# Optimization experiments

Measured on AMD Instinct MI355X. Metric: run time of the kernel, lower is better.

Reference implementation:

```python
import jax, jax.numpy as jnp
import numpy as np

CHUNK = 512  # tile size along N; keeps per-step [B,CHUNK,M] tile ~64 MB, never builds full [B,N,M]


def setup_inputs() -> dict:
    key = jax.random.key(0)
    k1, k2 = jax.random.split(key)
    xyz1 = jax.random.normal(k1, (4, 8192, 3), dtype=jnp.float32)
    xyz2 = jax.random.normal(k2, (4, 8192, 3), dtype=jnp.float32)
    return {"xyz1": xyz1, "xyz2": xyz2}


def _chamfer(xyz1, xyz2):
    # xyz1: [B,N,3], xyz2: [B,M,3]
    B, N, _ = xyz1.shape
    M = xyz2.shape[1]
    K = N // CHUNK
    x1_chunks = xyz1.reshape(B, K, CHUNK, 3).transpose(1, 0, 2, 3)  # [K,B,C,3]

    def step(carry, x1k):
        best_d2, best_i2, start = carry  # running mins for xyz2 -> xyz1 direction
        # squared distances for this tile: [B,C,M]
        d = jnp.sum((x1k[:, :, None, :] - xyz2[:, None, :, :]) ** 2, axis=-1)
        # xyz1 -> xyz2: min over M
        d1 = jnp.min(d, axis=2)                              # [B,C]
        i1 = jnp.argmin(d, axis=2).astype(jnp.int32)         # [B,C]
        # xyz2 -> xyz1: partial min over this chunk of N
        dc = jnp.min(d, axis=1)                              # [B,M]
        ic = jnp.argmin(d, axis=1).astype(jnp.int32) + start # [B,M], global index
        upd = dc < best_d2
        best_d2 = jnp.where(upd, dc, best_d2)
        best_i2 = jnp.where(upd, ic, best_i2)
        return (best_d2, best_i2, start + CHUNK), (d1, i1)

    init = (jnp.full((B, M), jnp.inf, dtype=xyz1.dtype),
            jnp.zeros((B, M), dtype=jnp.int32),
            jnp.int32(0))
    (dist2, idx2, _), (d1s, i1s) = jax.lax.scan(step, init, x1_chunks)
    dist1 = d1s.transpose(1, 0, 2).reshape(B, N)
    idx1 = i1s.transpose(1, 0, 2).reshape(B, N)
    return dist1, dist2, idx1, idx2


def reference(xyz1, xyz2):
    # Matches ChamferDistance.forward: (dist1, dist2, idx1, idx2),
    # squared nearest-neighbor distances and int32 argmin indices.
    return _chamfer(xyz1, xyz2)
```

## Files before the change

### kernel.cpp

```cpp
#include <hip/hip_runtime.h>
#include <math.h>


#define QPT 4
#define BLK 256
#define QPB (QPT*BLK)

#define LOADF8(J) do {                                                        \
    f0 = sv4[8*(J)+0]; f1 = sv4[8*(J)+1]; f2 = sv4[8*(J)+2];                  \
    f3 = sv4[8*(J)+3]; f4 = sv4[8*(J)+4]; f5 = sv4[8*(J)+5];                  \
    f6 = sv4[8*(J)+6]; f7 = sv4[8*(J)+7];                                     \
} while (0)

#define EMIN8(AX, AY, AZ, MOUT) do {                                          \
    float d0 = fmaf(AX, f0.x, fmaf(AY, f0.y, fmaf(AZ, f0.z, f0.w)));          \
    float d1 = fmaf(AX, f1.x, fmaf(AY, f1.y, fmaf(AZ, f1.z, f1.w)));          \
    float d2 = fmaf(AX, f2.x, fmaf(AY, f2.y, fmaf(AZ, f2.z, f2.w)));          \
    float d3 = fmaf(AX, f3.x, fmaf(AY, f3.y, fmaf(AZ, f3.z, f3.w)));          \
    float d4 = fmaf(AX, f4.x, fmaf(AY, f4.y, fmaf(AZ, f4.z, f4.w)));          \
    float d5 = fmaf(AX, f5.x, fmaf(AY, f5.y, fmaf(AZ, f5.z, f5.w)));          \
    float d6 = fmaf(AX, f6.x, fmaf(AY, f6.y, fmaf(AZ, f6.z, f6.w)));          \
    float d7 = fmaf(AX, f7.x, fmaf(AY, f7.y, fmaf(AZ, f7.z, f7.w)));          \
    float t0 = fminf(fminf(d0, d1), d2);                                      \
    float t1 = fminf(fminf(d3, d4), d5);                                      \
    float t2 = fminf(fminf(d6, d7), t0);                                      \
    MOUT = fminf(t1, t2);                                                     \
} while (0)

#define DMIN8(QX, QY, QZ, MOUT) do {                                          \
    float dx, dy, dz;                                                         \
    dx = QX - f0.x; dy = QY - f0.y; dz = QZ - f0.z;                           \
    float d0 = fmaf(dx, dx, fmaf(dy, dy, dz * dz));                           \
    dx = QX - f1.x; dy = QY - f1.y; dz = QZ - f1.z;                           \
    float d1 = fmaf(dx, dx, fmaf(dy, dy, dz * dz));                           \
    dx = QX - f2.x; dy = QY - f2.y; dz = QZ - f2.z;                           \
    float d2 = fmaf(dx, dx, fmaf(dy, dy, dz * dz));                           \
    dx = QX - f3.x; dy = QY - f3.y; dz = QZ - f3.z;                           \
    float d3 = fmaf(dx, dx, fmaf(dy, dy, dz * dz));                           \
    dx = QX - f4.x; dy = QY - f4.y; dz = QZ - f4.z;                           \
    float d4 = fmaf(dx, dx, fmaf(dy, dy, dz * dz));                           \
    dx = QX - f5.x; dy = QY - f5.y; dz = QZ - f5.z;                           \
    float d5 = fmaf(dx, dx, fmaf(dy, dy, dz * dz));                           \
    dx = QX - f6.x; dy = QY - f6.y; dz = QZ - f6.z;                           \
    float d6 = fmaf(dx, dx, fmaf(dy, dy, dz * dz));                           \
    dx = QX - f7.x; dy = QY - f7.y; dz = QZ - f7.z;                           \
    float d7 = fmaf(dx, dx, fmaf(dy, dy, dz * dz));                           \
    float t0 = fminf(fminf(d0, d1), d2);                                      \
    float t1 = fminf(fminf(d3, d4), d5);                                      \
    float t2 = fminf(fminf(d6, d7), t0);                                      \
    MOUT = fminf(t1, t2);                                                     \
} while (0)

__global__ __launch_bounds__(256, 4) void chamfer_main(
    const float* __restrict__ xyz1, const float* __restrict__ xyz2,
    unsigned long long* __restrict__ pp,
    int N, int M, int B, int S, int C)
{
    const int dir = blockIdx.z;
    const float* q = dir ? xyz2 : xyz1;
    const float* r = dir ? xyz1 : xyz2;
    const int Nq = dir ? M : N;
    const int Nr = dir ? N : M;
    const int b     = blockIdx.y / S;
    const int split = blockIdx.y % S;
    const int base  = split * C;

    extern __shared__ float s[];
    float4* sv4 = (float4*)s;

    {
        const float* g3 = r + ((size_t)b * Nr + base) * 3;
        for (int t = threadIdx.x; t < C; t += BLK) {
            float gx = g3[3 * t + 0];
            float gy = g3[3 * t + 1];
            float gz = g3[3 * t + 2];
            float rr = fmaf(gz, gz, fmaf(gy, gy, gx * gx));
            float4 f; f.x = gx; f.y = gy; f.z = gz; f.w = rr;
            sv4[t] = f;
        }
    }
    __syncthreads();

    float ax[QPT], ay[QPT], az[QPT];
    int qi[QPT];
    bool qvv[QPT];
#pragma unroll
    for (int k = 0; k < QPT; ++k) {
        qi[k] = blockIdx.x * QPB + k * BLK + threadIdx.x;
        qvv[k] = qi[k] < Nq;
        const float* qp = q + ((size_t)b * Nq + (qvv[k] ? qi[k] : 0)) * 3;
        ax[k] = -2.0f * qp[0]; ay[k] = -2.0f * qp[1]; az[k] = -2.0f * qp[2];
    }

    float e1[QPT], e2[QPT];
    int   g1[QPT];
#pragma unroll
    for (int k = 0; k < QPT; ++k) { e1[k] = INFINITY; e2[k] = INFINITY; g1[k] = 0; }

    const int iters = C / 8;
    for (int j8 = 0; j8 < iters; ++j8) {
        float4 f0, f1, f2, f3, f4, f5, f6, f7;
        LOADF8(j8);
#pragma unroll
        for (int k = 0; k < QPT; ++k) {
            float m;
            EMIN8(ax[k], ay[k], az[k], m);
            float h = fmaxf(e1[k], m);
            e2[k] = fminf(e2[k], h);
            if (m < e1[k]) g1[k] = j8;
            e1[k] = fminf(e1[k], m);
        }
    }

    const size_t obase = (size_t)(dir * B + b) * Nq;
    const int gbase = split * (C / 8);
#pragma unroll
    for (int k = 0; k < QPT; ++k) {
        if (!qvv[k]) continue;
        const float qx = -0.5f * ax[k], qy = -0.5f * ay[k], qz = -0.5f * az[k];
        int gi = g1[k];
        float dwin;
        bool resolved = false;
        {
            float qq  = fmaf(qx, qx, fmaf(qy, qy, qz * qz));
            float d1e = qq + e1[k];
            float rt  = sqrtf(qq) + sqrtf(fmaxf(d1e, 0.0f) + 0.01f);
            float eps = 4e-6f * fmaf(2.0f, rt * rt, qq);
            if (e2[k] - e1[k] <= eps) {
                const float lim = e1[k] + eps;
                unsigned long long mask = 0ull;
                for (int j8 = 0; j8 < iters; ++j8) {
                    float4 f0, f1, f2, f3, f4, f5, f6, f7;
                    LOADF8(j8);
                    float m;
                    EMIN8(ax[k], ay[k], az[k], m);
                    if (m <= lim) mask |= 1ull << j8;
                }
                float bdx = INFINITY; int gs = 0;
                for (int j8 = 0; j8 < iters; ++j8) {
                    if (!((mask >> j8) & 1)) continue;
                    float4 f0, f1, f2, f3, f4, f5, f6, f7;
                    LOADF8(j8);
                    float md;
                    DMIN8(qx, qy, qz, md);
                    if (md < bdx) { bdx = md; gs = j8; }
                }
                gi = gs; dwin = bdx; resolved = true;
            }
        }
        if (!resolved) {
            const float4* rv =
                (const float4*)(r + ((size_t)b * Nr + base + (size_t)gi * 8) * 3);
            float4 h0 = rv[0], h1 = rv[1], h2 = rv[2],
                   h3 = rv[3], h4 = rv[4], h5 = rv[5];
            float px[8] = { h0.x, h0.w, h1.z, h2.y, h3.x, h3.w, h4.z, h5.y };
            float py[8] = { h0.y, h1.x, h1.w, h2.z, h3.y, h4.x, h4.w, h5.z };
            float pz[8] = { h0.z, h1.y, h2.x, h2.w, h3.z, h4.y, h5.x, h5.w };
            float d[8];
#pragma unroll
            for (int p = 0; p < 8; ++p) {
                float dx = qx - px[p];
                float dy = qy - py[p];
                float dz = qz - pz[p];
                d[p] = fmaf(dx, dx, fmaf(dy, dy, dz * dz));
            }
            float t0 = fminf(fminf(d[0], d[1]), d[2]);
            float t1 = fminf(fminf(d[3], d[4]), d[5]);
            float t2 = fminf(fminf(d[6], d[7]), t0);
            dwin = fminf(t1, t2);
        }
        unsigned long long packed =
            ((unsigned long long)__float_as_uint(dwin) << 32)
            | (unsigned)(gbase + gi);
        atomicMin(&pp[obase + qi[k]], packed);
    }
}

__global__ __launch_bounds__(256) void chamfer_final(
    const float* __restrict__ xyz1, const float* __restrict__ xyz2,
    const unsigned long long* __restrict__ pp,
    float* __restrict__ out, int N, int M, int B)
{
    const int gid = blockIdx.x * blockDim.x + threadIdx.x;
    const int perDir0 = B * N;
    int dir, rem;
    if (gid < perDir0) { dir = 0; rem = gid; }
    else if (gid < perDir0 + B * M) { dir = 1; rem = gid - perDir0; }
    else return;
    const int Nq = dir ? M : N;
    const int Nr = dir ? N : M;
    const float* q = dir ? xyz2 : xyz1;
    const float* r = dir ? xyz1 : xyz2;

    unsigned long long v = pp[(size_t)(dir * B) * Nq + rem];
    const unsigned bits = (unsigned)(v >> 32);
    const int grp = (int)(v & 0xffffffffu);

    const int b  = rem / Nq;
    const int qi = rem - b * Nq;
    const float* qp = q + ((size_t)b * Nq + qi) * 3;
    const float qx = qp[0], qy = qp[1], qz = qp[2];

    const float4* rv = (const float4*)(r + ((size_t)b * Nr + (size_t)grp * 8) * 3);
    float4 f0 = rv[0], f1 = rv[1], f2 = rv[2], f3 = rv[3], f4 = rv[4], f5 = rv[5];
    float px[8] = { f0.x, f0.w, f1.z, f2.y, f3.x, f3.w, f4.z, f5.y };
    float py[8] = { f0.y, f1.x, f1.w, f2.z, f3.y, f4.x, f4.w, f5.z };
    float pz[8] = { f0.z, f1.y, f2.x, f2.w, f3.z, f4.y, f5.x, f5.w };
    int best = 0;
#pragma unroll
    for (int p = 7; p >= 0; --p) {
        float dx = qx - px[p];
        float dy = qy - py[p];
        float dz = qz - pz[p];
        float d = fmaf(dx, dx, fmaf(dy, dy, dz * dz));
        if (__float_as_uint(d) == bits) best = p;
    }
    const int idx = grp * 8 + best;

    float* dist_out = out + (dir ? (size_t)B * N : 0);
    float* idx_out  = out + (size_t)B * N + (size_t)B * M + (dir ? (size_t)B * N : 0);
    dist_out[rem] = __uint_as_float(bits);
    idx_out[rem]  = (float)idx;
}

extern "C" void kernel_launch(void* const* d_in, const int* in_sizes, int n_in,
                              void* d_out, int out_size, void* d_ws, size_t ws_size,
                              hipStream_t stream) {
    const float* xyz1 = (const float*)d_in[0];
    const float* xyz2 = (const float*)d_in[1];
    float* out = (float*)d_out;
    const int B = 4;
    const int N = in_sizes[0] / (B * 3);
    const int M = in_sizes[1] / (B * 3);
    const int NQ = (N > M ? N : M);
    const int NR = (N > M ? N : M);

    int S = 32;
    while (NR % (S * 8)) S >>= 1;
    const int C = NR / S;

    unsigned long long* pp = (unsigned long long*)d_ws;
    const int nslots = 2 * B * NQ;

    hipMemsetAsync(pp, 0xFF, (size_t)nslots * 8, stream);

    dim3 grid((NQ + QPB - 1) / QPB, B * S, 2);
    size_t lds = (size_t)C * 4 * sizeof(float);
    chamfer_main<<<grid, dim3(BLK, 1, 1), lds, stream>>>(
        xyz1, xyz2, pp, N, M, B, S, C);

    chamfer_final<<<dim3((nslots + 255) / 256, 1, 1), dim3(256, 1, 1), 0, stream>>>(
        xyz1, xyz2, pp, out, N, M, B);
}
```

Baseline: 120.2 us.

## Precompute augmented point array once and read reference points from global memory

Adds a prep kernel that writes every point as a float4 (x, y, z, |p|^2) into workspace. The main kernel then reads the reference points straight from that global array instead of staging them through LDS. This is meant to remove the per-block LDS fill, the block barrier and the repeated norm computation, and to raise occupancy by using no LDS. In exchange every wave issues uniform global loads that depend on cache hits, and there is an extra kernel launch. The old LDS path is kept as a fallback when the workspace is too small.

```diff
diff --git a/kernel.cpp b/kernel.cpp
--- a/kernel.cpp
+++ b/kernel.cpp
@@ -5,12 +5,6 @@
 #define QPT 4
 #define BLK 256
 #define QPB (QPT*BLK)
-
-#define LOADF8(J) do {                                                        \
-    f0 = sv4[8*(J)+0]; f1 = sv4[8*(J)+1]; f2 = sv4[8*(J)+2];                  \
-    f3 = sv4[8*(J)+3]; f4 = sv4[8*(J)+4]; f5 = sv4[8*(J)+5];                  \
-    f6 = sv4[8*(J)+6]; f7 = sv4[8*(J)+7];                                     \
-} while (0)
 
 #define EMIN8(AX, AY, AZ, MOUT) do {                                          \
     float d0 = fmaf(AX, f0.x, fmaf(AY, f0.y, fmaf(AZ, f0.z, f0.w)));          \
@@ -51,7 +45,141 @@
     MOUT = fminf(t1, t2);                                                     \
 } while (0)
 
-__global__ __launch_bounds__(256, 4) void chamfer_main(
+__global__ __launch_bounds__(256) void chamfer_prep(
+    const float* __restrict__ xyz1, const float* __restrict__ xyz2,
+    float4* __restrict__ aug, int n1, int total)
+{
+    const int i = blockIdx.x * blockDim.x + threadIdx.x;
+    if (i >= total) return;
+    const float* src = (i < n1) ? (xyz1 + 3 * (size_t)i)
+                                : (xyz2 + 3 * (size_t)(i - n1));
+    float gx = src[0], gy = src[1], gz = src[2];
+    float rr = fmaf(gz, gz, fmaf(gy, gy, gx * gx));
+    float4 f; f.x = gx; f.y = gy; f.z = gz; f.w = rr;
+    aug[i] = f;
+}
+
+__global__ __launch_bounds__(256, 4) void chamfer_main_aug(
+    const float* __restrict__ xyz1, const float* __restrict__ xyz2,
+    const float4* __restrict__ aug,
+    unsigned long long* __restrict__ pp,
+    int N, int M, int B, int S, int C)
+{
+    const int dir = blockIdx.z;
+    const float* q = dir ? xyz2 : xyz1;
+    const int Nq = dir ? M : N;
+    const int Nr = dir ? N : M;
+    const int b     = blockIdx.y / S;
+    const int split = blockIdx.y % S;
+    const int base  = split * C;
+
+    const float4* ag = aug + (dir ? 0 : (size_t)B * N) + (size_t)b * Nr + base;
+
+    float ax[QPT], ay[QPT], az[QPT];
+    int qi[QPT];
+    bool qvv[QPT];
+#pragma unroll
+    for (int k = 0; k < QPT; ++k) {
+        qi[k] = blockIdx.x * QPB + k * BLK + threadIdx.x;
+        qvv[k] = qi[k] < Nq;
+        const float* qp = q + ((size_t)b * Nq + (qvv[k] ? qi[k] : 0)) * 3;
+        ax[k] = -2.0f * qp[0]; ay[k] = -2.0f * qp[1]; az[k] = -2.0f * qp[2];
+    }
+
+    float e1[QPT], e2[QPT];
+    int   g1[QPT];
+#pragma unroll
+    for (int k = 0; k < QPT; ++k) { e1[k] = INFINITY; e2[k] = INFINITY; g1[k] = 0; }
+
+    const int iters = C / 8;
+    for (int j8 = 0; j8 < iters; ++j8) {
+        const float4 f0 = ag[8 * j8 + 0];
+        const float4 f1 = ag[8 * j8 + 1];
+        const float4 f2 = ag[8 * j8 + 2];
+        const float4 f3 = ag[8 * j8 + 3];
+        const float4 f4 = ag[8 * j8 + 4];
+        const float4 f5 = ag[8 * j8 + 5];
+        const float4 f6 = ag[8 * j8 + 6];
+        const float4 f7 = ag[8 * j8 + 7];
+#pragma unroll
+        for (int k = 0; k < QPT; ++k) {
+            float m;
+            EMIN8(ax[k], ay[k], az[k], m);
+            float h = fmaxf(e1[k], m);
+            e2[k] = fminf(e2[k], h);
+            if (m < e1[k]) g1[k] = j8;
+            e1[k] = fminf(e1[k], m);
+        }
+    }
+
+    const size_t obase = (size_t)(dir * B + b) * Nq;
+    const int gbase = split * (C / 8);
+#pragma unroll
+    for (int k = 0; k < QPT; ++k) {
+        if (!qvv[k]) continue;
+        const float qx = -0.5f * ax[k], qy = -0.5f * ay[k], qz = -0.5f * az[k];
+        int gi = g1[k];
+        float dwin;
+        bool resolved = false;
+        {
+            float qq  = fmaf(qx, qx, fmaf(qy, qy, qz * qz));
+            float d1e = qq + e1[k];
+            float rt  = sqrtf(qq) + sqrtf(fmaxf(d1e, 0.0f) + 0.01f);
+            float eps = 4e-6f * fmaf(2.0f, rt * rt, qq);
+            if (e2[k] - e1[k] <= eps) {
+                const float lim = e1[k] + eps;
+                unsigned long long mask = 0ull;
+                for (int j8 = 0; j8 < iters; ++j8) {
+                    const float4 f0 = ag[8 * j8 + 0];
+                    const float4 f1 = ag[8 * j8 + 1];
+                    const float4 f2 = ag[8 * j8 + 2];
+                    const float4 f3 = ag[8 * j8 + 3];
+                    const float4 f4 = ag[8 * j8 + 4];
+                    const float4 f5 = ag[8 * j8 + 5];
+                    const float4 f6 = ag[8 * j8 + 6];
+                    const float4 f7 = ag[8 * j8 + 7];
+                    float m;
+                    EMIN8(ax[k], ay[k], az[k], m);
+                    if (m <= lim) mask |= 1ull << j8;
+                }
+                float bdx = INFINITY; int gs = 0;
+                for (int j8 = 0; j8 < iters; ++j8) {
+                    if (!((mask >> j8) & 1)) continue;
+                    const float4 f0 = ag[8 * j8 + 0];
+                    const float4 f1 = ag[8 * j8 + 1];
+                    const float4 f2 = ag[8 * j8 + 2];
+                    const float4 f3 = ag[8 * j8 + 3];
+                    const float4 f4 = ag[8 * j8 + 4];
+                    const float4 f5 = ag[8 * j8 + 5];
+                    const float4 f6 = ag[8 * j8 + 6];
+                    const float4 f7 = ag[8 * j8 + 7];
+                    float md;
+                    DMIN8(qx, qy, qz, md);
+                    if (md < bdx) { bdx = md; gs = j8; }
+                }
+                gi = gs; dwin = bdx; resolved = true;
+            }
+        }
+        if (!resolved) {
+            const float4* gv = ag + (size_t)gi * 8;
+            const float4 f0 = gv[0], f1 = gv[1], f2 = gv[2], f3 = gv[3],
+                         f4 = gv[4], f5 = gv[5], f6 = gv[6], f7 = gv[7];
+            DMIN8(qx, qy, qz, dwin);
+        }
+        unsigned long long packed =
+            ((unsigned long long)__float_as_uint(dwin) << 32)
+            | (unsigned)(gbase + gi);
+        atomicMin(&pp[obase + qi[k]], packed);
+    }
+}
+
+#define LOADF8(J) do {                                                        \
+    f0 = sv4[8*(J)+0]; f1 = sv4[8*(J)+1]; f2 = sv4[8*(J)+2];                  \
+    f3 = sv4[8*(J)+3]; f4 = sv4[8*(J)+4]; f5 = sv4[8*(J)+5];                  \
+    f6 = sv4[8*(J)+6]; f7 = sv4[8*(J)+7];                                     \
+} while (0)
+
+__global__ __launch_bounds__(256, 4) void chamfer_main_lds(
     const float* __restrict__ xyz1, const float* __restrict__ xyz2,
     unsigned long long* __restrict__ pp,
     int N, int M, int B, int S, int C)
@@ -67,13 +195,10 @@
 
     extern __shared__ float s[];
     float4* sv4 = (float4*)s;
-
     {
         const float* g3 = r + ((size_t)b * Nr + base) * 3;
         for (int t = threadIdx.x; t < C; t += BLK) {
-            float gx = g3[3 * t + 0];
-            float gy = g3[3 * t + 1];
-            float gz = g3[3 * t + 2];
+            float gx = g3[3 * t + 0], gy = g3[3 * t + 1], gz = g3[3 * t + 2];
             float rr = fmaf(gz, gz, fmaf(gy, gy, gx * gx));
             float4 f; f.x = gx; f.y = gy; f.z = gz; f.w = rr;
             sv4[t] = f;
@@ -91,7 +216,6 @@
         const float* qp = q + ((size_t)b * Nq + (qvv[k] ? qi[k] : 0)) * 3;
         ax[k] = -2.0f * qp[0]; ay[k] = -2.0f * qp[1]; az[k] = -2.0f * qp[2];
     }
-
     float e1[QPT], e2[QPT];
     int   g1[QPT];
 #pragma unroll
@@ -241,13 +365,24 @@
 
     unsigned long long* pp = (unsigned long long*)d_ws;
     const int nslots = 2 * B * NQ;
-
-    hipMemsetAsync(pp, 0xFF, (size_t)nslots * 8, stream);
+    const size_t ppBytes  = (size_t)nslots * 8;
+    const size_t augElems = (size_t)B * N + (size_t)B * M;
+    const size_t needed   = ppBytes + augElems * sizeof(float4);
+
+    hipMemsetAsync(pp, 0xFF, ppBytes, stream);
 
     dim3 grid((NQ + QPB - 1) / QPB, B * S, 2);
-    size_t lds = (size_t)C * 4 * sizeof(float);
-    chamfer_main<<<grid, dim3(BLK, 1, 1), lds, stream>>>(
-        xyz1, xyz2, pp, N, M, B, S, C);
+    if (ws_size >= needed) {
+        float4* aug = (float4*)((char*)d_ws + ppBytes);
+        chamfer_prep<<<dim3((augElems + 255) / 256, 1, 1), dim3(256, 1, 1), 0,
+                       stream>>>(xyz1, xyz2, aug, B * N, (int)augElems);
+        chamfer_main_aug<<<grid, dim3(BLK, 1, 1), 0, stream>>>(
+            xyz1, xyz2, aug, pp, N, M, B, S, C);
+    } else {
+        size_t lds = (size_t)C * 4 * sizeof(float);
+        chamfer_main_lds<<<grid, dim3(BLK, 1, 1), lds, stream>>>(
+            xyz1, xyz2, pp, N, M, B, S, C);
+    }
 
     chamfer_final<<<dim3((nslots + 255) / 256, 1, 1), dim3(256, 1, 1), 0, stream>>>(
         xyz1, xyz2, pp, out, N, M, B);
```

New measurement: 137.3 us. +14.3%, slower.
